# Kernel tuning notes

Measured on AMD Instinct MI355X. Metric: run time of the kernel, lower is better.

Reference implementation:

```python
import jax, jax.numpy as jnp
import numpy as np

N_HEAD = 16
TEMPERATURE = 1.0

def setup_inputs() -> dict:
    key = jax.random.key(0)
    ks = jax.random.split(key, 5)
    B, L, D = 2, 2048, 1024
    s = 0.02
    return {
        'x':     jax.random.normal(ks[0], (B, L, D), jnp.float32),
        'q_g':   jax.random.normal(ks[1], (B, L, D), jnp.float32),
        'k_g':   jax.random.normal(ks[2], (B, L, D), jnp.float32),
        'W_qkv': jax.random.normal(ks[3], (D, 3 * D), jnp.float32) * s,
        'W_out': jax.random.normal(ks[4], (D, D), jnp.float32) * s,
    }

def reference(x, q_g, k_g, W_qkv, W_out):
    B, L, D = x.shape
    H = N_HEAD
    hd = D // H
    qkv = x @ W_qkv                                    # [B, L, 3D]
    q, k, v = jnp.split(qkv, 3, axis=-1)
    def to_heads(t):                                    # [B,L,D] -> [B,H,L,hd]
        return t.reshape(B, L, H, hd).transpose(0, 2, 1, 3)
    q, k, v = to_heads(q), to_heads(k), to_heads(v)
    qg, kg = to_heads(q_g), to_heads(k_g)

    scale = 1.0 / jnp.sqrt(jnp.float32(hd))
    # dual score matrices (same math as concat-on-head-dim then split)
    aw_x = jnp.einsum('bhqd,bhkd->bhqk', q, k) * scale    # [B,H,L,L]
    aw_g = jnp.einsum('bhqd,bhkd->bhqk', qg, kg) * scale  # [B,H,L,L]
    # sensory_attention=True, merge='add'
    attn = aw_x + aw_g

    causal = jnp.tril(jnp.ones((L, L), dtype=bool))
    attn = jnp.where(causal, attn, -jnp.inf)
    log_norm = jnp.log(jnp.float32(L))                    # softmax_log_norm=True
    attn = jax.nn.softmax(attn / (log_norm * TEMPERATURE), axis=-1)

    y = jnp.einsum('bhqk,bhkd->bhqd', attn, v)            # [B,H,L,hd]
    y = y.transpose(0, 2, 1, 3).reshape(B, L, D)
    return y @ W_out
```

## Files before the change

### kernel.cpp

```cpp
#include <hip/hip_runtime.h>

typedef __attribute__((ext_vector_type(8))) short bf16x8;
typedef __attribute__((ext_vector_type(4))) float f32x4;

static __device__ __forceinline__ unsigned short f2bf(float f) {
    unsigned int u = __float_as_uint(f);
    u += 0x7fffu + ((u >> 16) & 1u);
    return (unsigned short)(u >> 16);
}
static __device__ __forceinline__ unsigned int pack2bf(float lo, float hi) {
    return ((__float_as_uint(lo) + 0x8000u) >> 16) |
           ((__float_as_uint(hi) + 0x8000u) & 0xffff0000u);
}
static __device__ __forceinline__ float bf2f(short v) {
    return __uint_as_float(((unsigned int)(unsigned short)v) << 16);
}
static __device__ __forceinline__ bf16x8 cvt8v(const float* p) {
    f32x4 a = *(const f32x4*)p, b = *(const f32x4*)(p + 4);
    bf16x8 r;
    r[0] = (short)f2bf(a[0]); r[1] = (short)f2bf(a[1]);
    r[2] = (short)f2bf(a[2]); r[3] = (short)f2bf(a[3]);
    r[4] = (short)f2bf(b[0]); r[5] = (short)f2bf(b[1]);
    r[6] = (short)f2bf(b[2]); r[7] = (short)f2bf(b[3]);
    return r;
}
static __device__ __forceinline__ bf16x8 scale8v(bf16x8 v, float s) {
    bf16x8 r;
    #pragma unroll
    for (int j = 0; j < 8; ++j) r[j] = (short)f2bf(bf2f(v[j]) * s);
    return r;
}
static __device__ __forceinline__ uint4 cvt8(const float* p) {
    bf16x8 r = cvt8v(p);
    union { bf16x8 v; uint4 u; } c; c.v = r; return c.u;
}
static __device__ __forceinline__ void glds16(const unsigned short* g, unsigned short* l) {
    __builtin_amdgcn_global_load_lds(
        (const __attribute__((address_space(1))) unsigned int*)g,
        (__attribute__((address_space(3))) unsigned int*)l, 16, 0, 0);
}

static __device__ __forceinline__ void transpose_tile(
    const float* __restrict__ src, unsigned short* __restrict__ dst,
    int R, int C, int bx, int by, int tid)
{
    __shared__ unsigned short t[64 * 72];
    const int r0 = by * 64, c0 = bx * 64;
    #pragma unroll
    for (int i = 0; i < 4; ++i) {
        int idx = tid + i * 256;
        int row = idx >> 4, seg = idx & 15;
        f32x4 v = *(const f32x4*)&src[(size_t)(r0 + row) * C + c0 + seg * 4];
        #pragma unroll
        for (int j = 0; j < 4; ++j) t[row * 72 + seg * 4 + j] = f2bf(v[j]);
    }
    __syncthreads();
    #pragma unroll
    for (int i = 0; i < 2; ++i) {
        int idx = tid + i * 256;
        int row = idx >> 3, seg = idx & 7;
        uint4 tv; unsigned short* tmp = (unsigned short*)&tv;
        #pragma unroll
        for (int j = 0; j < 8; ++j) tmp[j] = t[(seg * 8 + j) * 72 + row];
        *(uint4*)&dst[(size_t)(c0 + row) * R + r0 + seg * 8] = tv;
    }
}

__global__ __launch_bounds__(256) void prep_all(
    const float* __restrict__ x, unsigned short* __restrict__ x_bf,
    const float* __restrict__ kg, unsigned short* __restrict__ kg_bf,
    const float* __restrict__ Wq, unsigned short* __restrict__ wtq,
    const float* __restrict__ Wo, unsigned short* __restrict__ wto)
{
    const int t = blockIdx.x, tid = threadIdx.x;
    if (t < 2048) {
        size_t j = ((size_t)t * 256 + tid) * 8;
        *(uint4*)&x_bf[j] = cvt8(&x[j]);
    } else if (t < 4096) {
        size_t j = ((size_t)(t - 2048) * 256 + tid) * 8;
        *(uint4*)&kg_bf[j] = cvt8(&kg[j]);
    } else if (t < 4864) {
        int tt = t - 4096;
        transpose_tile(Wq, wtq, 1024, 3072, tt % 48, tt / 48, tid);
    } else {
        int tt = t - 4864;
        transpose_tile(Wo, wto, 1024, 1024, tt & 15, tt >> 4, tid);
    }
}

__global__ __launch_bounds__(256) void gemm_qkv(
    const unsigned short* __restrict__ A, const unsigned short* __restrict__ Bt,
    unsigned short* __restrict__ qk, unsigned short* __restrict__ vt)
{
    const int K = 1024;
    __shared__ unsigned short As[128 * 32];
    __shared__ unsigned short Bs[128 * 32];
    __shared__ unsigned short Tb[128 * 136];
    const int tid = threadIdx.x;
    const int wave = tid >> 6, lane = tid & 63, quad = lane >> 4, l16 = lane & 15;
    const int wr = (wave >> 1) * 64, wc = (wave & 1) * 64;
    const int m0 = blockIdx.y * 128, n0 = blockIdx.x * 128;

    const unsigned short* ga = A  + (size_t)(m0 + wave * 32 + (lane >> 2)) * K + (lane & 3) * 8;
    const unsigned short* gb = Bt + (size_t)(n0 + wave * 32 + (lane >> 2)) * K + (lane & 3) * 8;
    unsigned short* la = &As[wave * 32 * 32];
    unsigned short* lb = &Bs[wave * 32 * 32];
    const size_t step16 = (size_t)16 * K;

    f32x4 acc[4][4];
    #pragma unroll
    for (int i = 0; i < 4; ++i)
        #pragma unroll
        for (int j = 0; j < 4; ++j) acc[i][j] = (f32x4){0.f, 0.f, 0.f, 0.f};

    for (int kt = 0; kt < K; kt += 32) {
        glds16(ga, la); glds16(ga + step16, la + 512);
        glds16(gb, lb); glds16(gb + step16, lb + 512);
        ga += 32; gb += 32;
        __syncthreads();
        bf16x8 af[4], bf[4];
        #pragma unroll
        for (int i = 0; i < 4; ++i) {
            af[i] = *(const bf16x8*)&As[(wr + i * 16 + l16) * 32 + quad * 8];
            bf[i] = *(const bf16x8*)&Bs[(wc + i * 16 + l16) * 32 + quad * 8];
        }
        #pragma unroll
        for (int mi = 0; mi < 4; ++mi)
            #pragma unroll
            for (int ni = 0; ni < 4; ++ni)
                acc[mi][ni] = __builtin_amdgcn_mfma_f32_16x16x32_bf16(
                    af[mi], bf[ni], acc[mi][ni], 0, 0, 0);
        __syncthreads();
    }

    if (blockIdx.x < 16) {
        #pragma unroll
        for (int mi = 0; mi < 4; ++mi)
            #pragma unroll
            for (int ni = 0; ni < 4; ++ni)
                #pragma unroll
                for (int r = 0; r < 4; ++r) {
                    int row = m0 + wr + mi * 16 + quad * 4 + r;
                    int col = n0 + wc + ni * 16 + l16;
                    qk[(size_t)row * 2048 + col] = f2bf(acc[mi][ni][r]);
                }
    } else {
        __syncthreads();
        #pragma unroll
        for (int mi = 0; mi < 4; ++mi)
            #pragma unroll
            for (int ni = 0; ni < 4; ++ni)
                #pragma unroll
                for (int r = 0; r < 4; ++r) {
                    int col = wc + ni * 16 + l16;
                    int row = wr + mi * 16 + quad * 4 + r;
                    Tb[col * 136 + row] = f2bf(acc[mi][ni][r]);
                }
        __syncthreads();
        const int col = tid >> 1, r0 = (tid & 1) * 64;
        const int bh = (m0 >> 11) * 16 + ((int)blockIdx.x - 16) * 2 + (col >> 6);
        size_t base = ((size_t)bh * 64 + (col & 63)) * 2048 + (m0 & 2047) + r0;
        #pragma unroll
        for (int k = 0; k < 8; ++k)
            *(uint4*)&vt[base + k * 8] = *(const uint4*)&Tb[col * 136 + r0 + k * 8];
    }
}

__global__ __launch_bounds__(256) void gemm_n64(
    const unsigned short* __restrict__ A, const unsigned short* __restrict__ Bt,
    float* __restrict__ C)
{
    const int K = 1024, N = 1024;
    __shared__ unsigned short As[128 * 32];
    __shared__ unsigned short Bs[64 * 32];
    const int tid = threadIdx.x;
    const int wave = tid >> 6, lane = tid & 63, quad = lane >> 4, l16 = lane & 15;
    const int wr = (wave >> 1) * 64, wc = (wave & 1) * 32;
    const int m0 = blockIdx.y * 128, n0 = blockIdx.x * 64;

    const unsigned short* ga = A  + (size_t)(m0 + wave * 32 + (lane >> 2)) * K + (lane & 3) * 8;
    const unsigned short* gb = Bt + (size_t)(n0 + wave * 16 + (lane >> 2)) * K + (lane & 3) * 8;
    unsigned short* la = &As[wave * 32 * 32];
    unsigned short* lb = &Bs[wave * 16 * 32];
    const size_t step16 = (size_t)16 * K;

    f32x4 acc[4][2];
    #pragma unroll
    for (int i = 0; i < 4; ++i)
        #pragma unroll
        for (int j = 0; j < 2; ++j) acc[i][j] = (f32x4){0.f, 0.f, 0.f, 0.f};

    for (int kt = 0; kt < K; kt += 32) {
        glds16(ga, la); glds16(ga + step16, la + 512);
        glds16(gb, lb);
        ga += 32; gb += 32;
        __syncthreads();
        bf16x8 af[4], bf[2];
        #pragma unroll
        for (int i = 0; i < 4; ++i)
            af[i] = *(const bf16x8*)&As[(wr + i * 16 + l16) * 32 + quad * 8];
        #pragma unroll
        for (int i = 0; i < 2; ++i)
            bf[i] = *(const bf16x8*)&Bs[(wc + i * 16 + l16) * 32 + quad * 8];
        #pragma unroll
        for (int mi = 0; mi < 4; ++mi)
            #pragma unroll
            for (int ni = 0; ni < 2; ++ni)
                acc[mi][ni] = __builtin_amdgcn_mfma_f32_16x16x32_bf16(
                    af[mi], bf[ni], acc[mi][ni], 0, 0, 0);
        __syncthreads();
    }
    #pragma unroll
    for (int mi = 0; mi < 4; ++mi)
        #pragma unroll
        for (int ni = 0; ni < 2; ++ni)
            #pragma unroll
            for (int r = 0; r < 4; ++r) {
                int row = m0 + wr + mi * 16 + quad * 4 + r;
                int col = n0 + wc + ni * 16 + l16;
                C[(size_t)row * N + col] = acc[mi][ni][r];
            }
}

__global__ __launch_bounds__(256, 5) void attn7(
    const unsigned short* __restrict__ qk, const float* __restrict__ qg,
    const unsigned short* __restrict__ kgb, const unsigned short* __restrict__ vt,
    unsigned short* __restrict__ y)
{
    const int L = 2048, DS = 2048, Dm = 1024;
    const float SC2 = 0.125f * 1.44269504088896f / 7.6246189861593985f;

    const int qt = 31 - (int)blockIdx.y;
    const int bh = blockIdx.x, b = bh >> 4, h = bh & 15;
    const int tid = threadIdx.x, wave = tid >> 6, lane = tid & 63;
    const int quad = lane >> 4, l16 = lane & 15;

    __shared__ unsigned short K_l[4096];
    __shared__ unsigned short G_l[4096];
    __shared__ unsigned short V_l[4096];
    __shared__ unsigned short P_l[4096];
    unsigned short* Pw = &P_l[wave * 1024];

    bf16x8 qf[2], gf[2];
    {
        const int qrow = qt * 64 + wave * 16 + l16;
        const unsigned short* qp = qk + (size_t)(b * L + qrow) * DS + h * 64;
        const float* gp = qg + (size_t)(b * L + qrow) * Dm + h * 64;
        #pragma unroll
        for (int c = 0; c < 2; ++c) {
            qf[c] = scale8v(*(const bf16x8*)(qp + c * 32 + quad * 8), SC2);
            gf[c] = scale8v(cvt8v(gp + c * 32 + quad * 8), SC2);
        }
    }

    f32x4 o[4];
    #pragma unroll
    for (int nd = 0; nd < 4; ++nd) o[nd] = (f32x4){0.f, 0.f, 0.f, 0.f};
    float lsum = 0.f;

    const int srow = wave * 16 + (lane >> 3);
    const int c8 = (((lane & 7) ^ (lane >> 3)) & 7) * 8;
    const unsigned short* pk = qk + (size_t)(b * L + srow) * DS + 1024 + h * 64 + c8;
    const unsigned short* pg = kgb + (size_t)(b * L + srow) * Dm + h * 64 + c8;
    const unsigned short* pv = vt + ((size_t)bh * 64 + srow) * L + c8;
    unsigned short* lK = &K_l[wave * 1024];
    unsigned short* lG = &G_l[wave * 1024];
    unsigned short* lV = &V_l[wave * 1024];

    const int rb = l16 * 128;
    const int swz0 = ((quad     ^ (l16 & 7)) * 16);
    const int swz1 = (((4 + quad) ^ (l16 & 7)) * 16);
    const int pwb = l16 * 64 + (quad & 1) * 4;
    const int pwc = quad >> 1, pxr = l16 & 7;

    for (int kt = 0; kt < qt; ++kt) {
        __syncthreads();
        glds16(pk, lK); glds16(pk + 8 * DS, lK + 512);
        glds16(pg, lG); glds16(pg + 8 * Dm, lG + 512);
        glds16(pv, lV); glds16(pv + 8 * L,  lV + 512);
        pk += 64 * DS; pg += 64 * Dm; pv += 64;
        __syncthreads();

        #pragma unroll
        for (int ni = 0; ni < 4; ++ni) {
            bf16x8 kf0 = *(const bf16x8*)((const char*)K_l + rb + swz0 + ni * 2048);
            bf16x8 kf1 = *(const bf16x8*)((const char*)K_l + rb + swz1 + ni * 2048);
            bf16x8 gb0 = *(const bf16x8*)((const char*)G_l + rb + swz0 + ni * 2048);
            bf16x8 gb1 = *(const bf16x8*)((const char*)G_l + rb + swz1 + ni * 2048);
            f32x4 a = (f32x4){0.f, 0.f, 0.f, 0.f};
            a = __builtin_amdgcn_mfma_f32_16x16x32_bf16(kf0, qf[0], a, 0, 0, 0);
            a = __builtin_amdgcn_mfma_f32_16x16x32_bf16(gb0, gf[0], a, 0, 0, 0);
            a = __builtin_amdgcn_mfma_f32_16x16x32_bf16(kf1, qf[1], a, 0, 0, 0);
            a = __builtin_amdgcn_mfma_f32_16x16x32_bf16(gb1, gf[1], a, 0, 0, 0);
            float e0 = exp2f(a[0]), e1 = exp2f(a[1]);
            float e2 = exp2f(a[2]), e3 = exp2f(a[3]);
            lsum += (e0 + e1) + (e2 + e3);
            unsigned int p01 = pack2bf(e0, e1), p23 = pack2bf(e2, e3);
            *(unsigned long long*)&Pw[pwb + (((ni * 2 + pwc) ^ pxr) * 8)] =
                ((unsigned long long)p23 << 32) | p01;
        }
        asm volatile("s_waitcnt lgkmcnt(0)" ::: "memory");

        bf16x8 pa[2];
        #pragma unroll
        for (int c = 0; c < 2; ++c)
            pa[c] = *(const bf16x8*)&Pw[l16 * 64 + (((c * 4 + quad) ^ pxr) * 8)];
        #pragma unroll
        for (int nd = 0; nd < 4; ++nd) {
            bf16x8 vf0 = *(const bf16x8*)((const char*)V_l + rb + swz0 + nd * 2048);
            bf16x8 vf1 = *(const bf16x8*)((const char*)V_l + rb + swz1 + nd * 2048);
            o[nd] = __builtin_amdgcn_mfma_f32_16x16x32_bf16(pa[0], vf0, o[nd], 0, 0, 0);
            o[nd] = __builtin_amdgcn_mfma_f32_16x16x32_bf16(pa[1], vf1, o[nd], 0, 0, 0);
        }
    }

    {
        __syncthreads();
        glds16(pk, lK); glds16(pk + 8 * DS, lK + 512);
        glds16(pg, lG); glds16(pg + 8 * Dm, lG + 512);
        glds16(pv, lV); glds16(pv + 8 * L,  lV + 512);
        __syncthreads();

        #pragma unroll
        for (int ni = 0; ni < 4; ++ni) {
            if (ni > wave) {
                *(unsigned long long*)&Pw[pwb + (((ni * 2 + pwc) ^ pxr) * 8)] = 0ull;
                continue;
            }
            bf16x8 kf0 = *(const bf16x8*)((const char*)K_l + rb + swz0 + ni * 2048);
            bf16x8 kf1 = *(const bf16x8*)((const char*)K_l + rb + swz1 + ni * 2048);
            bf16x8 gb0 = *(const bf16x8*)((const char*)G_l + rb + swz0 + ni * 2048);
            bf16x8 gb1 = *(const bf16x8*)((const char*)G_l + rb + swz1 + ni * 2048);
            f32x4 a = (f32x4){0.f, 0.f, 0.f, 0.f};
            a = __builtin_amdgcn_mfma_f32_16x16x32_bf16(kf0, qf[0], a, 0, 0, 0);
            a = __builtin_amdgcn_mfma_f32_16x16x32_bf16(gb0, gf[0], a, 0, 0, 0);
            a = __builtin_amdgcn_mfma_f32_16x16x32_bf16(kf1, qf[1], a, 0, 0, 0);
            a = __builtin_amdgcn_mfma_f32_16x16x32_bf16(gb1, gf[1], a, 0, 0, 0);
            float e0, e1, e2, e3;
            if (ni < wave) {
                e0 = exp2f(a[0]); e1 = exp2f(a[1]);
                e2 = exp2f(a[2]); e3 = exp2f(a[3]);
            } else {
                e0 = (quad * 4 + 0 <= l16) ? exp2f(a[0]) : 0.f;
                e1 = (quad * 4 + 1 <= l16) ? exp2f(a[1]) : 0.f;
                e2 = (quad * 4 + 2 <= l16) ? exp2f(a[2]) : 0.f;
                e3 = (quad * 4 + 3 <= l16) ? exp2f(a[3]) : 0.f;
            }
            lsum += (e0 + e1) + (e2 + e3);
            unsigned int p01 = pack2bf(e0, e1), p23 = pack2bf(e2, e3);
            *(unsigned long long*)&Pw[pwb + (((ni * 2 + pwc) ^ pxr) * 8)] =
                ((unsigned long long)p23 << 32) | p01;
        }
        asm volatile("s_waitcnt lgkmcnt(0)" ::: "memory");

        bf16x8 pa[2];
        #pragma unroll
        for (int c = 0; c < 2; ++c)
            pa[c] = *(const bf16x8*)&Pw[l16 * 64 + (((c * 4 + quad) ^ pxr) * 8)];
        #pragma unroll
        for (int nd = 0; nd < 4; ++nd) {
            bf16x8 vf0 = *(const bf16x8*)((const char*)V_l + rb + swz0 + nd * 2048);
            bf16x8 vf1 = *(const bf16x8*)((const char*)V_l + rb + swz1 + nd * 2048);
            o[nd] = __builtin_amdgcn_mfma_f32_16x16x32_bf16(pa[0], vf0, o[nd], 0, 0, 0);
            o[nd] = __builtin_amdgcn_mfma_f32_16x16x32_bf16(pa[1], vf1, o[nd], 0, 0, 0);
        }
    }

    float rs = lsum;
    rs += __shfl_xor(rs, 16);
    rs += __shfl_xor(rs, 32);
    #pragma unroll
    for (int r = 0; r < 4; ++r) {
        float inv = 1.f / __shfl(rs, (lane & 48) | (quad * 4 + r));
        int row = qt * 64 + wave * 16 + quad * 4 + r;
        #pragma unroll
        for (int nd = 0; nd < 4; ++nd)
            y[(size_t)(b * L + row) * Dm + h * 64 + nd * 16 + l16] =
                f2bf(o[nd][r] * inv);
    }
}

extern "C" void kernel_launch(void* const* d_in, const int* in_sizes, int n_in,
                              void* d_out, int out_size, void* d_ws, size_t ws_size,
                              hipStream_t stream) {
    const float* x     = (const float*)d_in[0];
    const float* q_g   = (const float*)d_in[1];
    const float* k_g   = (const float*)d_in[2];
    const float* W_qkv = (const float*)d_in[3];
    const float* W_out = (const float*)d_in[4];
    float* out = (float*)d_out;
    unsigned short* ws = (unsigned short*)d_ws;

    unsigned short* qk_ws = ws;
    unsigned short* y_ws  = ws + 8388608;
    unsigned short* wtq   = ws + 12582912;
    unsigned short* wto   = ws + 15728640;
    unsigned short* kg_bf = ws + 16777216;
    unsigned short* x_bf  = ws + 20971520;
    unsigned short* vt_bf = ws + 25165824;

    dim3 blk(256);
    prep_all<<<5120, blk, 0, stream>>>(x, x_bf, k_g, kg_bf, W_qkv, wtq, W_out, wto);
    gemm_qkv<<<dim3(24, 32), blk, 0, stream>>>(x_bf, wtq, qk_ws, vt_bf);
    attn7<<<dim3(32, 32), blk, 0, stream>>>(qk_ws, q_g, kg_bf, vt_bf, y_ws);
    gemm_n64<<<dim3(16, 32), blk, 0, stream>>>(y_ws, wto, out);
}
```

Before: 225.1 us.

## Split long causal query tiles across two blocks and combine partial outputs

The attention kernel now splits the KV loop of the 16 longest causal query tiles into two halves, each handled by its own block. Partial unnormalized outputs and row sums go to float workspace buffers, and a new combine kernel adds the halves, normalizes and writes bf16 y. This is meant to balance the causal workload and shorten the tail where the longest tiles dominate. It costs an extra kernel launch, extra global traffic for the partials, and workspace regions reused by aliasing buffers whose earlier contents are no longer needed.

```diff
diff --git a/kernel.cpp b/kernel.cpp
--- a/kernel.cpp
+++ b/kernel.cpp
@@ -222,15 +222,25 @@
             }
 }
 
-__global__ __launch_bounds__(256, 5) void attn7(
+__global__ __launch_bounds__(256, 5) void attn13(
     const unsigned short* __restrict__ qk, const float* __restrict__ qg,
     const unsigned short* __restrict__ kgb, const unsigned short* __restrict__ vt,
-    unsigned short* __restrict__ y)
+    unsigned short* __restrict__ y,
+    float* __restrict__ po0, float* __restrict__ po1,
+    float* __restrict__ ls0, float* __restrict__ ls1)
 {
     const int L = 2048, DS = 2048, Dm = 1024;
     const float SC2 = 0.125f * 1.44269504088896f / 7.6246189861593985f;
 
-    const int qt = 31 - (int)blockIdx.y;
+    const int yb = (int)blockIdx.y;
+    const bool isH1 = (yb < 16);
+    const bool isSplit = (yb < 32);
+    const int qt = isH1 ? (31 - yb) : (47 - yb);
+    const int ht = (qt + 1) >> 1;
+    const int nfull = isSplit ? (isH1 ? qt - ht : ht) : qt;
+    const bool dodiag = !isSplit || isH1;
+    const int kt0 = (isSplit && isH1) ? ht : 0;
+
     const int bh = blockIdx.x, b = bh >> 4, h = bh & 15;
     const int tid = threadIdx.x, wave = tid >> 6, lane = tid & 63;
     const int quad = lane >> 4, l16 = lane & 15;
@@ -260,9 +270,9 @@
 
     const int srow = wave * 16 + (lane >> 3);
     const int c8 = (((lane & 7) ^ (lane >> 3)) & 7) * 8;
-    const unsigned short* pk = qk + (size_t)(b * L + srow) * DS + 1024 + h * 64 + c8;
-    const unsigned short* pg = kgb + (size_t)(b * L + srow) * Dm + h * 64 + c8;
-    const unsigned short* pv = vt + ((size_t)bh * 64 + srow) * L + c8;
+    const unsigned short* pk = qk + (size_t)(b * L + kt0 * 64 + srow) * DS + 1024 + h * 64 + c8;
+    const unsigned short* pg = kgb + (size_t)(b * L + kt0 * 64 + srow) * Dm + h * 64 + c8;
+    const unsigned short* pv = vt + ((size_t)bh * 64 + srow) * L + kt0 * 64 + c8;
     unsigned short* lK = &K_l[wave * 1024];
     unsigned short* lG = &G_l[wave * 1024];
     unsigned short* lV = &V_l[wave * 1024];
@@ -273,7 +283,7 @@
     const int pwb = l16 * 64 + (quad & 1) * 4;
     const int pwc = quad >> 1, pxr = l16 & 7;
 
-    for (int kt = 0; kt < qt; ++kt) {
+    for (int kt = 0; kt < nfull; ++kt) {
         __syncthreads();
         glds16(pk, lK); glds16(pk + 8 * DS, lK + 512);
         glds16(pg, lG); glds16(pg + 8 * Dm, lG + 512);
@@ -314,7 +324,7 @@
         }
     }
 
-    {
+    if (dodiag) {
         __syncthreads();
         glds16(pk, lK); glds16(pk + 8 * DS, lK + 512);
         glds16(pg, lG); glds16(pg + 8 * Dm, lG + 512);
@@ -369,14 +379,59 @@
     float rs = lsum;
     rs += __shfl_xor(rs, 16);
     rs += __shfl_xor(rs, 32);
-    #pragma unroll
-    for (int r = 0; r < 4; ++r) {
-        float inv = 1.f / __shfl(rs, (lane & 48) | (quad * 4 + r));
-        int row = qt * 64 + wave * 16 + quad * 4 + r;
-        #pragma unroll
-        for (int nd = 0; nd < 4; ++nd)
-            y[(size_t)(b * L + row) * Dm + h * 64 + nd * 16 + l16] =
-                f2bf(o[nd][r] * inv);
+
+    if (isSplit) {
+        const int pair = bh * 16 + (qt - 16);
+        float* po = (isH1 ? po1 : po0) + (size_t)pair * 4096;
+        float* pls = (isH1 ? ls1 : ls0) + (size_t)pair * 64;
+        #pragma unroll
+        for (int r = 0; r < 4; ++r) {
+            int row = wave * 16 + quad * 4 + r;
+            #pragma unroll
+            for (int nd = 0; nd < 4; ++nd)
+                po[row * 64 + nd * 16 + l16] = o[nd][r];
+        }
+        if (lane < 16) pls[wave * 16 + lane] = rs;
+    } else {
+        #pragma unroll
+        for (int r = 0; r < 4; ++r) {
+            float inv = 1.f / __shfl(rs, (lane & 48) | (quad * 4 + r));
+            int row = qt * 64 + wave * 16 + quad * 4 + r;
+            #pragma unroll
+            for (int nd = 0; nd < 4; ++nd)
+                y[(size_t)(b * L + row) * Dm + h * 64 + nd * 16 + l16] =
+                    f2bf(o[nd][r] * inv);
+        }
+    }
+}
+
+__global__ __launch_bounds__(256) void attn_combine(
+    const float* __restrict__ po0, const float* __restrict__ po1,
+    const float* __restrict__ ls0, const float* __restrict__ ls1,
+    unsigned short* __restrict__ y)
+{
+    const int pair = blockIdx.x;
+    const int bh = pair >> 4, qt = (pair & 15) + 16;
+    const int b = bh >> 4, h = bh & 15;
+    const int tid = threadIdx.x;
+    const int r = tid >> 2, c0 = (tid & 3) * 16;
+
+    __shared__ float inv[64];
+    if (tid < 64) inv[tid] = 1.f / (ls0[pair * 64 + tid] + ls1[pair * 64 + tid]);
+    __syncthreads();
+
+    const float* p0 = po0 + (size_t)pair * 4096 + r * 64 + c0;
+    const float* p1 = po1 + (size_t)pair * 4096 + r * 64 + c0;
+    unsigned short* yp = y + (size_t)(b * 2048 + qt * 64 + r) * 1024 + h * 64 + c0;
+    const float s = inv[r];
+    #pragma unroll
+    for (int j = 0; j < 4; ++j) {
+        f32x4 a = *(const f32x4*)(p0 + j * 4);
+        f32x4 c = *(const f32x4*)(p1 + j * 4);
+        yp[j * 4 + 0] = f2bf((a[0] + c[0]) * s);
+        yp[j * 4 + 1] = f2bf((a[1] + c[1]) * s);
+        yp[j * 4 + 2] = f2bf((a[2] + c[2]) * s);
+        yp[j * 4 + 3] = f2bf((a[3] + c[3]) * s);
     }
 }
 
@@ -394,14 +449,20 @@
     unsigned short* qk_ws = ws;
     unsigned short* y_ws  = ws + 8388608;
     unsigned short* wtq   = ws + 12582912;
-    unsigned short* wto   = ws + 15728640;
     unsigned short* kg_bf = ws + 16777216;
     unsigned short* x_bf  = ws + 20971520;
     unsigned short* vt_bf = ws + 25165824;
+    unsigned short* wto   = ws + 29360128;
+    float* po0 = (float*)(ws + 20971520);
+    float* po1 = (float*)(ws + 12582912);
+    float* ls0 = (float*)(ws + 30408704);
+    float* ls1 = (float*)(ws + 30474240);
 
     dim3 blk(256);
     prep_all<<<5120, blk, 0, stream>>>(x, x_bf, k_g, kg_bf, W_qkv, wtq, W_out, wto);
     gemm_qkv<<<dim3(24, 32), blk, 0, stream>>>(x_bf, wtq, qk_ws, vt_bf);
-    attn7<<<dim3(32, 32), blk, 0, stream>>>(qk_ws, q_g, kg_bf, vt_bf, y_ws);
+    attn13<<<dim3(32, 48), blk, 0, stream>>>(qk_ws, q_g, kg_bf, vt_bf, y_ws,
+                                             po0, po1, ls0, ls1);
+    attn_combine<<<512, blk, 0, stream>>>(po0, po1, ls0, ls1, y_ws);
     gemm_n64<<<dim3(16, 32), blk, 0, stream>>>(y_ws, wto, out);
 }
```

Measured after the change: 227.0 us. Within noise of the previous version (+0.8%).
